# Kernel optimization log

Measured on AMD Instinct MI355X. Metric: run time of the kernel, lower is better.

## Reference

```python
import jax, jax.numpy as jnp
import numpy as np
import math

H = 128          # num heads
D = 5120         # hidden
Q_LORA = 1536
KV_LORA = 512    # nope_size / latent dim
ROPE = 64        # qk_rope_head_dim
NOPE = 128       # qk_nope_head_dim
VDIM = 128       # v_head_dim
Q_HEAD = NOPE + ROPE  # 192
EPS = 1e-6
_MSCALE = 0.1 * 1.0 * math.log(40.0) + 1.0
SCALE = (Q_HEAD ** -0.5) * _MSCALE * _MSCALE


def rmsnorm(x, w):
    var = jnp.mean(x.astype(jnp.float32) ** 2, axis=-1, keepdims=True)
    return (x * jax.lax.rsqrt(var + EPS)).astype(x.dtype) * w


def rotate_half(x):
    h = x.shape[-1] // 2
    return jnp.concatenate([-x[..., h:], x[..., :h]], axis=-1)


def apply_rope(x, cos, sin):
    return x * cos + rotate_half(x) * sin


def setup_inputs() -> dict:
    key = jax.random.key(0)
    ks = jax.random.split(key, 12)
    S = 1024
    s = 0.02
    return {
        'hidden_states': jax.random.normal(ks[0], (1, S, D), jnp.float32),
        'cos': jax.random.uniform(ks[1], (S, ROPE), jnp.float32, -1.0, 1.0),
        'sin': jax.random.uniform(ks[2], (S, ROPE), jnp.float32, -1.0, 1.0),
        'q_a_w': jax.random.normal(ks[3], (D, Q_LORA), jnp.float32) * s,
        'q_a_ln_w': jnp.ones((Q_LORA,), jnp.float32),
        'q_b_w': jax.random.normal(ks[4], (Q_LORA, H * Q_HEAD), jnp.float32) * s,
        'kv_a_w': jax.random.normal(ks[5], (D, KV_LORA + ROPE), jnp.float32) * s,
        'kv_a_ln_w': jnp.ones((KV_LORA,), jnp.float32),
        'kc_w': jax.random.normal(ks[6], (H, NOPE, KV_LORA), jnp.float32) * s,
        'vc_w': jax.random.normal(ks[7], (H, KV_LORA, VDIM), jnp.float32) * s,
        'o_w': jax.random.normal(ks[8], (H * VDIM, D), jnp.float32) * s,
    }


def reference(hidden_states, cos, sin, q_a_w, q_a_ln_w, q_b_w, kv_a_w,
              kv_a_ln_w, kc_w, vc_w, o_w):
    h = hidden_states[0]                     # [S, D]
    S = h.shape[0]

    # --- q path: low-rank q with RMSNorm, then absorbed nope proj via per-head bmm
    q = rmsnorm(h @ q_a_w, q_a_ln_w) @ q_b_w  # [S, H*192]
    q = q.reshape(S, H, Q_HEAD)
    q_nope, q_pe = q[..., :NOPE], q[..., NOPE:]         # [S,H,128], [S,H,64]
    q_nope_abs = jnp.einsum('shd,hdl->shl', q_nope, kc_w)  # [S,H,512] (kc bmm)

    # --- kv path: shared latent (MQA, 1 kv head)
    kv = h @ kv_a_w                          # [S, 512+64]
    k_pe = kv[:, KV_LORA:]                   # [S, 64]
    latent = rmsnorm(kv[:, :KV_LORA], kv_a_ln_w)  # [S, 512] = value states

    # --- partial RoPE on the 64-dim pe slice only
    q_pe = apply_rope(q_pe, cos[:, None, :], sin[:, None, :])
    k_pe = apply_rope(k_pe, cos, sin)

    q_full = jnp.concatenate([q_nope_abs, q_pe], axis=-1)  # [S,H,576]
    k_full = jnp.concatenate([latent, k_pe], axis=-1)      # [S,576]

    # --- causal MLA attention in latent space (values = 512-dim latent)
    scores = jnp.einsum('qhd,kd->hqk', q_full, k_full) * SCALE  # [H,S,S]
    causal = jnp.tril(jnp.ones((S, S), bool))
    scores = jnp.where(causal[None], scores, jnp.finfo(scores.dtype).min)
    probs = jax.nn.softmax(scores, axis=-1)
    attn = jnp.einsum('hqk,kl->qhl', probs, latent)         # [S,H,512]

    # --- vc bmm back to v_head_dim, then output proj
    out = jnp.einsum('shl,hlv->shv', attn, vc_w)            # [S,H,128]
    out = out.reshape(S, H * VDIM) @ o_w                    # [S, D]
    return out[None]                                        # [1,S,D]
```

## Files before the change

kernel.cpp:

```cpp
#include <hip/hip_runtime.h>
#include <hip/hip_bf16.h>
#include <math.h>

#define S_LEN  1024
#define DMODEL 5120
#define QLORA  1536
#define KVLORA 512
#define ROPE_D 64
#define NOPE_D 128
#define VDIM_D 128
#define QHEAD  192
#define NHEAD  128

typedef __hip_bfloat16 bf16;

using bf16x8 = __attribute__((ext_vector_type(8))) __bf16;
using f32x4  = __attribute__((ext_vector_type(4))) float;

__device__ __forceinline__ float toF(float x) { return x; }
__device__ __forceinline__ float toF(bf16 x)  { return __bfloat162float(x); }

__device__ __forceinline__ bf16x8 ld8(const bf16* p) {
  return *reinterpret_cast<const bf16x8*>(p);
}

__global__ __launch_bounds__(256) void cvt_bf16(const float* __restrict__ in,
                                                bf16* __restrict__ out) {
  const int i = (blockIdx.x * 256 + threadIdx.x) * 4;
  const float4 v = *reinterpret_cast<const float4*>(in + i);
  out[i + 0] = __float2bfloat16(v.x);
  out[i + 1] = __float2bfloat16(v.y);
  out[i + 2] = __float2bfloat16(v.z);
  out[i + 3] = __float2bfloat16(v.w);
}

__global__ __launch_bounds__(256) void transpose_w(const float* __restrict__ in,
                                                   bf16* __restrict__ out,
                                                   int R, int C) {
  __shared__ float tile[32][33];
  const int h = blockIdx.z;
  const int c0 = blockIdx.x * 32, r0 = blockIdx.y * 32;
  const int rr = threadIdx.x >> 3, cc = (threadIdx.x & 7) * 4;
  const float* ip = in + ((size_t)h * R + r0 + rr) * C + c0 + cc;
#pragma unroll
  for (int i = 0; i < 4; ++i) tile[rr][cc + i] = ip[i];
  __syncthreads();
  bf16* op = out + ((size_t)h * C + c0 + rr) * R + r0 + cc;
#pragma unroll
  for (int i = 0; i < 4; ++i) op[i] = __float2bfloat16(tile[cc + i][rr]);
}

template<int MODE, int SPLIT = 1>
__global__ __launch_bounds__(256) void gemm_mfma(const bf16* __restrict__ A,
                                                 const bf16* __restrict__ BT,
                                                 void* __restrict__ Cout,
                                                 int M, int N, int K) {
  __shared__ bf16 As[128][72];
  __shared__ bf16 Bs[128][72];
  const int n0 = blockIdx.x * 128, m0 = blockIdx.y * 128;
  const int z  = (SPLIT > 1) ? blockIdx.z : 0;
  const int Ks = K / SPLIT;
  const int kbeg = z * Ks;
  const int tid = threadIdx.x;
  const int w = tid >> 6, l = tid & 63, lr = l & 15, lg = l >> 4;
  const int wr = w >> 1, wc = w & 1;

  f32x4 acc[4][4];
#pragma unroll
  for (int x = 0; x < 4; ++x)
#pragma unroll
    for (int y = 0; y < 4; ++y) acc[x][y] = (f32x4){0.f, 0.f, 0.f, 0.f};

  for (int kk = kbeg; kk < kbeg + Ks; kk += 64) {
#pragma unroll
    for (int i = 0; i < 4; ++i) {
      const int e = tid + 256 * i;
      const int r = e >> 3, k8 = (e & 7) * 8;
      *reinterpret_cast<bf16x8*>(&As[r][k8]) =
          ld8(A + (size_t)(m0 + r) * K + kk + k8);
      const int bn = (n0 + r < N) ? n0 + r : N - 1;
      *reinterpret_cast<bf16x8*>(&Bs[r][k8]) =
          ld8(BT + (size_t)bn * K + kk + k8);
    }
    __syncthreads();
#pragma unroll
    for (int kh = 0; kh < 2; ++kh) {
      bf16x8 af[4], bg[4];
#pragma unroll
      for (int x = 0; x < 4; ++x) af[x] = ld8(&As[wr * 64 + x * 16 + lr][kh * 32 + lg * 8]);
#pragma unroll
      for (int y = 0; y < 4; ++y) bg[y] = ld8(&Bs[wc * 64 + y * 16 + lr][kh * 32 + lg * 8]);
#pragma unroll
      for (int x = 0; x < 4; ++x)
#pragma unroll
        for (int y = 0; y < 4; ++y)
          acc[x][y] = __builtin_amdgcn_mfma_f32_16x16x32_bf16(af[x], bg[y], acc[x][y], 0, 0, 0);
    }
    __syncthreads();
  }

#pragma unroll
  for (int x = 0; x < 4; ++x) {
    const int mb = m0 + wr * 64 + x * 16 + lg * 4;
#pragma unroll
    for (int y = 0; y < 4; ++y) {
      const int n = n0 + wc * 64 + y * 16 + lr;
      if (n < N) {
#pragma unroll
        for (int i = 0; i < 4; ++i) {
          const int m = mb + i;
          if (MODE == 0) {
            ((float*)Cout)[(size_t)m * N + n] = acc[x][y][i];
          } else if (MODE == 1) {
            ((bf16*)Cout)[(size_t)m * N + n] = __float2bfloat16(acc[x][y][i]);
          } else if (MODE == 2) {
            const int h = n / QHEAD, j = n - h * QHEAD;
            ((bf16*)Cout)[((size_t)h * S_LEN + m) * QHEAD + j] = __float2bfloat16(acc[x][y][i]);
          } else {
            ((float*)Cout)[(size_t)z * M * N + (size_t)m * N + n] = acc[x][y][i];
          }
        }
      }
    }
  }
}

__global__ __launch_bounds__(256) void rmsnorm_fused(const float* __restrict__ part,
                                                     const float* __restrict__ w,
                                                     bf16* __restrict__ out) {
  const int row = blockIdx.x, tid = threadIdx.x;
  __shared__ float red[256];
  float x[6];
  float ss = 0.f;
#pragma unroll
  for (int j = 0; j < 6; ++j) {
    const int c = tid + 256 * j;
    float s = 0.f;
#pragma unroll
    for (int z = 0; z < 8; ++z) s += part[((size_t)z * S_LEN + row) * QLORA + c];
    x[j] = s; ss += s * s;
  }
  red[tid] = ss; __syncthreads();
  for (int t = 128; t > 0; t >>= 1) { if (tid < t) red[tid] += red[tid + t]; __syncthreads(); }
  const float rs = rsqrtf(red[0] / (float)QLORA + 1e-6f);
#pragma unroll
  for (int j = 0; j < 6; ++j) {
    const int c = tid + 256 * j;
    out[(size_t)row * QLORA + c] = __float2bfloat16(x[j] * rs * w[c]);
  }
}

__global__ __launch_bounds__(256) void kfull_fused(const float* __restrict__ part,
                                                   const float* __restrict__ w,
                                                   const float* __restrict__ cosb,
                                                   const float* __restrict__ sinb,
                                                   bf16* __restrict__ kfull) {
  const int s = blockIdx.x, tid = threadIdx.x;
  __shared__ float red[256];
  float x0 = 0.f, x1 = 0.f;
#pragma unroll
  for (int z = 0; z < 16; ++z) {
    const float* row = part + ((size_t)z * S_LEN + s) * 576;
    x0 += row[tid]; x1 += row[256 + tid];
  }
  red[tid] = x0 * x0 + x1 * x1; __syncthreads();
  for (int t = 128; t > 0; t >>= 1) { if (tid < t) red[tid] += red[tid + t]; __syncthreads(); }
  const float rs = rsqrtf(red[0] / 512.f + 1e-6f);
  bf16* krow = kfull + (size_t)s * 576;
  krow[tid]       = __float2bfloat16(x0 * rs * w[tid]);
  krow[256 + tid] = __float2bfloat16(x1 * rs * w[256 + tid]);
  if (tid < 32) {
    const int j = tid;
    float a = 0.f, b = 0.f;
#pragma unroll
    for (int z = 0; z < 16; ++z) {
      const float* row = part + ((size_t)z * S_LEN + s) * 576;
      a += row[512 + j]; b += row[544 + j];
    }
    const float* cs = cosb + (size_t)s * 64;
    const float* sn = sinb + (size_t)s * 64;
    krow[512 + j] = __float2bfloat16(a * cs[j] - b * sn[j]);
    krow[544 + j] = __float2bfloat16(b * cs[32 + j] + a * sn[32 + j]);
  }
}

__global__ __launch_bounds__(256) void reduce2_f32(const float* __restrict__ p,
                                                   float* __restrict__ out) {
  const size_t i = ((size_t)blockIdx.x * 256 + threadIdx.x) * 4;
  const float4 a = *reinterpret_cast<const float4*>(p + i);
  const float4 b = *reinterpret_cast<const float4*>(p + (size_t)S_LEN * DMODEL + i);
  float4 r; r.x = a.x + b.x; r.y = a.y + b.y; r.z = a.z + b.z; r.w = a.w + b.w;
  *reinterpret_cast<float4*>(out + i) = r;
}

__global__ __launch_bounds__(256) void rope_q_kernel(bf16* __restrict__ qperm,
                                                     const float* __restrict__ cosb,
                                                     const float* __restrict__ sinb) {
  const int idx = blockIdx.x * 256 + threadIdx.x;
  const int h = idx >> 15;
  const int rem = idx & 32767;
  const int s = rem >> 5;
  const int j = rem & 31;
  bf16* base = qperm + ((size_t)h * S_LEN + s) * QHEAD + NOPE_D;
  const float a = toF(base[j]), b = toF(base[32 + j]);
  const float* cs = cosb + (size_t)s * 64;
  const float* sn = sinb + (size_t)s * 64;
  base[j]      = __float2bfloat16(a * cs[j] - b * sn[j]);
  base[32 + j] = __float2bfloat16(b * cs[32 + j] + a * sn[32 + j]);
}

__global__ __launch_bounds__(256) void latT_kernel(const bf16* __restrict__ kfull,
                                                   bf16* __restrict__ latT) {
  const int gid = blockIdx.x * 256 + threadIdx.x;
  const int v = gid >> 10, s = gid & 1023;
  latT[gid] = kfull[(size_t)s * 576 + v];
}

#define QB 32
__global__ __launch_bounds__(256, 3) void attn_mfma(const bf16* __restrict__ qperm,
                                                    const bf16* __restrict__ kfull,
                                                    const bf16* __restrict__ kcT,
                                                    const bf16* __restrict__ vcT,
                                                    const bf16* __restrict__ latT,
                                                    bf16* __restrict__ attnv,
                                                    float scale) {
  const int bi = blockIdx.x;
  const int y  = bi >> 3;
  const int h  = (bi & 7) * 16 + (y >> 5);
  const int qb = y & 31;
  const int r0 = qb * QB;
  const int tid = threadIdx.x;
  const int w = tid >> 6, l = tid & 63, lr = l & 15, lg = l >> 4;

  __shared__ bf16  Qf[QB][584];
  __shared__ float St[QB][68];
  __shared__ bf16  Pt[QB][72];
  __shared__ float mrow[QB], lrow[QB], arow[QB];

  for (int e = tid; e < QB * 64; e += 256) {
    const int i = e >> 6, j = e & 63;
    Qf[i][512 + j] = qperm[((size_t)h * S_LEN + r0 + i) * QHEAD + NOPE_D + j];
  }
  {
    bf16x8 qn[2][4];
#pragma unroll
    for (int x = 0; x < 2; ++x) {
      const bf16* qp = qperm + ((size_t)h * S_LEN + r0 + x * 16 + lr) * QHEAD;
#pragma unroll
      for (int t = 0; t < 4; ++t) qn[x][t] = ld8(qp + t * 32 + lg * 8);
    }
#pragma unroll
    for (int ff = 0; ff < 2; ++ff) {
      bf16x8 kb[4][4];
#pragma unroll
      for (int f4 = 0; f4 < 4; ++f4) {
        const int col = w * 128 + (ff * 4 + f4) * 16 + lr;
        const bf16* kp = kcT + ((size_t)h * 512 + col) * 128 + lg * 8;
#pragma unroll
        for (int t = 0; t < 4; ++t) kb[f4][t] = ld8(kp + t * 32);
      }
#pragma unroll
      for (int f4 = 0; f4 < 4; ++f4) {
        f32x4 a0 = {0.f, 0.f, 0.f, 0.f}, a1 = {0.f, 0.f, 0.f, 0.f};
        const int col = w * 128 + (ff * 4 + f4) * 16 + lr;
#pragma unroll
        for (int t = 0; t < 4; ++t) {
          a0 = __builtin_amdgcn_mfma_f32_16x16x32_bf16(qn[0][t], kb[f4][t], a0, 0, 0, 0);
          a1 = __builtin_amdgcn_mfma_f32_16x16x32_bf16(qn[1][t], kb[f4][t], a1, 0, 0, 0);
        }
#pragma unroll
        for (int i = 0; i < 4; ++i) {
          Qf[lg * 4 + i][col]      = __float2bfloat16(a0[i]);
          Qf[16 + lg * 4 + i][col] = __float2bfloat16(a1[i]);
        }
      }
    }
  }
  if (tid < QB) { mrow[tid] = -INFINITY; lrow[tid] = 0.f; }
  __syncthreads();

  f32x4 o[2][8];
#pragma unroll
  for (int x = 0; x < 2; ++x)
#pragma unroll
    for (int f = 0; f < 8; ++f) o[x][f] = (f32x4){0.f, 0.f, 0.f, 0.f};

  const int kend = r0 + QB;
  for (int k0 = 0; k0 < kend; k0 += 64) {
    {
      const int key = k0 + w * 16 + lr;
      const bf16* kp = kfull + (size_t)key * 576 + lg * 8;
      bf16x8 bb[18];
#pragma unroll
      for (int t = 0; t < 18; ++t) bb[t] = ld8(kp + t * 32);
      f32x4 s0 = {0.f, 0.f, 0.f, 0.f}, s1 = {0.f, 0.f, 0.f, 0.f};
      __builtin_amdgcn_s_setprio(1);
#pragma unroll
      for (int t = 0; t < 18; ++t) {
        s0 = __builtin_amdgcn_mfma_f32_16x16x32_bf16(ld8(&Qf[lr][t * 32 + lg * 8]), bb[t], s0, 0, 0, 0);
        s1 = __builtin_amdgcn_mfma_f32_16x16x32_bf16(ld8(&Qf[16 + lr][t * 32 + lg * 8]), bb[t], s1, 0, 0, 0);
      }
      __builtin_amdgcn_s_setprio(0);
#pragma unroll
      for (int i = 0; i < 4; ++i) {
        const int q0 = r0 + lg * 4 + i;
        const int q1 = r0 + 16 + lg * 4 + i;
        St[lg * 4 + i][w * 16 + lr]      = (key <= q0) ? s0[i] * scale : -INFINITY;
        St[16 + lg * 4 + i][w * 16 + lr] = (key <= q1) ? s1[i] * scale : -INFINITY;
      }
    }
    __syncthreads();
    {
      const int r = tid >> 3, seg = tid & 7;
      const float4 v0 = *reinterpret_cast<const float4*>(&St[r][seg * 8]);
      const float4 v1 = *reinterpret_cast<const float4*>(&St[r][seg * 8 + 4]);
      float mx = fmaxf(fmaxf(fmaxf(v0.x, v0.y), fmaxf(v0.z, v0.w)),
                       fmaxf(fmaxf(v1.x, v1.y), fmaxf(v1.z, v1.w)));
#pragma unroll
      for (int m = 1; m < 8; m <<= 1) mx = fmaxf(mx, __shfl_xor(mx, m, 64));
      const float mold = mrow[r];
      const float mnew = fmaxf(mold, mx);
      const float p0 = expf(v0.x - mnew), p1 = expf(v0.y - mnew);
      const float p2 = expf(v0.z - mnew), p3 = expf(v0.w - mnew);
      const float p4 = expf(v1.x - mnew), p5 = expf(v1.y - mnew);
      const float p6 = expf(v1.z - mnew), p7 = expf(v1.w - mnew);
      Pt[r][seg * 8 + 0] = __float2bfloat16(p0);
      Pt[r][seg * 8 + 1] = __float2bfloat16(p1);
      Pt[r][seg * 8 + 2] = __float2bfloat16(p2);
      Pt[r][seg * 8 + 3] = __float2bfloat16(p3);
      Pt[r][seg * 8 + 4] = __float2bfloat16(p4);
      Pt[r][seg * 8 + 5] = __float2bfloat16(p5);
      Pt[r][seg * 8 + 6] = __float2bfloat16(p6);
      Pt[r][seg * 8 + 7] = __float2bfloat16(p7);
      float sum = p0 + p1 + p2 + p3 + p4 + p5 + p6 + p7;
#pragma unroll
      for (int m = 1; m < 8; m <<= 1) sum += __shfl_xor(sum, m, 64);
      if (seg == 0) {
        const float alpha = expf(mold - mnew);
        lrow[r] = lrow[r] * alpha + sum;
        mrow[r] = mnew;
        arow[r] = alpha;
      }
    }
    __syncthreads();
    {
      bf16x8 bl[16];
#pragma unroll
      for (int f = 0; f < 8; ++f) {
        const int v = w * 128 + f * 16 + lr;
        const bf16* bp = latT + (size_t)v * S_LEN + k0 + lg * 8;
        bl[2 * f]     = ld8(bp);
        bl[2 * f + 1] = ld8(bp + 32);
      }
      float al0[4], al1[4];
#pragma unroll
      for (int i = 0; i < 4; ++i) {
        al0[i] = arow[lg * 4 + i];
        al1[i] = arow[16 + lg * 4 + i];
      }
#pragma unroll
      for (int f = 0; f < 8; ++f)
#pragma unroll
        for (int i = 0; i < 4; ++i) {
          o[0][f][i] *= al0[i];
          o[1][f][i] *= al1[i];
        }
      bf16x8 pa[2][2];
      pa[0][0] = ld8(&Pt[lr][lg * 8]);
      pa[0][1] = ld8(&Pt[lr][32 + lg * 8]);
      pa[1][0] = ld8(&Pt[16 + lr][lg * 8]);
      pa[1][1] = ld8(&Pt[16 + lr][32 + lg * 8]);
      __builtin_amdgcn_s_setprio(1);
#pragma unroll
      for (int f = 0; f < 8; ++f) {
        o[0][f] = __builtin_amdgcn_mfma_f32_16x16x32_bf16(pa[0][0], bl[2 * f],     o[0][f], 0, 0, 0);
        o[0][f] = __builtin_amdgcn_mfma_f32_16x16x32_bf16(pa[0][1], bl[2 * f + 1], o[0][f], 0, 0, 0);
        o[1][f] = __builtin_amdgcn_mfma_f32_16x16x32_bf16(pa[1][0], bl[2 * f],     o[1][f], 0, 0, 0);
        o[1][f] = __builtin_amdgcn_mfma_f32_16x16x32_bf16(pa[1][1], bl[2 * f + 1], o[1][f], 0, 0, 0);
      }
      __builtin_amdgcn_s_setprio(0);
    }
  }

  {
    float li0[4], li1[4];
#pragma unroll
    for (int i = 0; i < 4; ++i) {
      li0[i] = 1.f / lrow[lg * 4 + i];
      li1[i] = 1.f / lrow[16 + lg * 4 + i];
    }
#pragma unroll
    for (int f = 0; f < 8; ++f) {
      const int v = w * 128 + f * 16 + lr;
#pragma unroll
      for (int i = 0; i < 4; ++i) {
        Qf[lg * 4 + i][v]      = __float2bfloat16(o[0][f][i] * li0[i]);
        Qf[16 + lg * 4 + i][v] = __float2bfloat16(o[1][f][i] * li1[i]);
      }
    }
  }
  __syncthreads();
#pragma unroll
  for (int cf = 0; cf < 2; ++cf) {
    const int c = w * 32 + cf * 16 + lr;
    const bf16* vp = vcT + ((size_t)h * 128 + c) * 512 + lg * 8;
    bf16x8 vb[16];
#pragma unroll
    for (int kt = 0; kt < 16; ++kt) vb[kt] = ld8(vp + kt * 32);
    f32x4 acc0 = {0.f, 0.f, 0.f, 0.f}, acc1 = {0.f, 0.f, 0.f, 0.f};
#pragma unroll
    for (int kt = 0; kt < 16; ++kt) {
      acc0 = __builtin_amdgcn_mfma_f32_16x16x32_bf16(ld8(&Qf[lr][kt * 32 + lg * 8]), vb[kt], acc0, 0, 0, 0);
      acc1 = __builtin_amdgcn_mfma_f32_16x16x32_bf16(ld8(&Qf[16 + lr][kt * 32 + lg * 8]), vb[kt], acc1, 0, 0, 0);
    }
#pragma unroll
    for (int i = 0; i < 4; ++i) {
      attnv[(size_t)(r0 + lg * 4 + i) * (NHEAD * VDIM_D) + h * VDIM_D + c]      = __float2bfloat16(acc0[i]);
      attnv[(size_t)(r0 + 16 + lg * 4 + i) * (NHEAD * VDIM_D) + h * VDIM_D + c] = __float2bfloat16(acc1[i]);
    }
  }
}

extern "C" void kernel_launch(void* const* d_in, const int* in_sizes, int n_in,
                              void* d_out, int out_size, void* d_ws, size_t ws_size,
                              hipStream_t stream) {
  const float* hidden    = (const float*)d_in[0];
  const float* cosb      = (const float*)d_in[1];
  const float* sinb      = (const float*)d_in[2];
  const float* q_a_w     = (const float*)d_in[3];
  const float* q_a_ln_w  = (const float*)d_in[4];
  const float* q_b_w     = (const float*)d_in[5];
  const float* kv_a_w    = (const float*)d_in[6];
  const float* kv_a_ln_w = (const float*)d_in[7];
  const float* kc_w      = (const float*)d_in[8];
  const float* vc_w      = (const float*)d_in[9];
  const float* o_w       = (const float*)d_in[10];
  float* out = (float*)d_out;

  char* ws = (char*)d_ws;
  bf16*  attnv   = (bf16*)(ws + 0);
  bf16*  kcT     = (bf16*)(ws + 33554432);
  bf16*  vcT     = (bf16*)(ws + 50331648);
  bf16*  kfull   = (bf16*)(ws + 67108864);
  bf16*  latT    = (bf16*)(ws + 68288512);
  bf16*  qan     = (bf16*)(ws + 69337088);
  bf16*  hb      = (bf16*)(ws + 72482816);
  bf16*  qaT     = (bf16*)(ws + 82968576);
  bf16*  kvaT    = (bf16*)(ws + 98697216);
  bf16*  qperm   = (bf16*)(ws + 104595456);
  float* qa_part = (float*)(ws + 104595456);
  bf16*  qbT     = (bf16*)(ws + 154927104);
  float* kv_part = (float*)(ws + 154927104);
  float* o_part  = (float*)(ws + 33554432);
  bf16*  owT     = (bf16*)(ws + 75497472);

  const double msc = 0.1 * log(40.0) + 1.0;
  const float scale = (float)(pow((double)QHEAD, -0.5) * msc * msc);

  cvt_bf16<<<(S_LEN * DMODEL) / 1024, 256, 0, stream>>>(hidden, hb);
  transpose_w<<<dim3(QLORA / 32, DMODEL / 32, 1), 256, 0, stream>>>(q_a_w, qaT, DMODEL, QLORA);
  transpose_w<<<dim3(576 / 32, DMODEL / 32, 1), 256, 0, stream>>>(kv_a_w, kvaT, DMODEL, 576);
  transpose_w<<<dim3((NHEAD * QHEAD) / 32, QLORA / 32, 1), 256, 0, stream>>>(q_b_w, qbT, QLORA, NHEAD * QHEAD);
  transpose_w<<<dim3(512 / 32, 128 / 32, NHEAD), 256, 0, stream>>>(kc_w, kcT, 128, 512);
  transpose_w<<<dim3(128 / 32, 512 / 32, NHEAD), 256, 0, stream>>>(vc_w, vcT, 512, 128);

  gemm_mfma<3, 8><<<dim3(QLORA / 128, S_LEN / 128, 8), 256, 0, stream>>>(
      hb, qaT, qa_part, S_LEN, QLORA, DMODEL);
  rmsnorm_fused<<<S_LEN, 256, 0, stream>>>(qa_part, q_a_ln_w, qan);
  gemm_mfma<2><<<dim3((NHEAD * QHEAD) / 128, S_LEN / 128), 256, 0, stream>>>(
      qan, qbT, qperm, S_LEN, NHEAD * QHEAD, QLORA);
  gemm_mfma<3, 16><<<dim3(5, S_LEN / 128, 16), 256, 0, stream>>>(
      hb, kvaT, kv_part, S_LEN, KVLORA + ROPE_D, DMODEL);
  kfull_fused<<<S_LEN, 256, 0, stream>>>(kv_part, kv_a_ln_w, cosb, sinb, kfull);
  latT_kernel<<<(KVLORA * S_LEN) / 256, 256, 0, stream>>>(kfull, latT);
  rope_q_kernel<<<(NHEAD * S_LEN * 32) / 256, 256, 0, stream>>>(qperm, cosb, sinb);
  attn_mfma<<<dim3(NHEAD * (S_LEN / QB)), 256, 0, stream>>>(
      qperm, kfull, kcT, vcT, latT, attnv, scale);
  transpose_w<<<dim3(DMODEL / 32, (NHEAD * VDIM_D) / 32, 1), 256, 0, stream>>>(
      o_w, owT, NHEAD * VDIM_D, DMODEL);
  gemm_mfma<3, 2><<<dim3(DMODEL / 128, S_LEN / 128, 2), 256, 0, stream>>>(
      attnv, owT, o_part, S_LEN, DMODEL, NHEAD * VDIM_D);
  reduce2_f32<<<(S_LEN * DMODEL) / 1024, 256, 0, stream>>>(o_part, out);
}
```

Before: 2.039 ms.

## Process 128 keys per softmax step and merge score/prob buffers in LDS

The attention loop now handles 128 keys per iteration (two 64-key score halves) before each online-softmax update, which halves the number of softmax passes and barrier pairs per key range. Probabilities are written back as fp32 into the score buffer and packed to bf16 at PV time, and the row statistics are stored in spare columns of that buffer. Latent values are loaded in 32-key chunks with early exit at the causal boundary. The cost is a larger LDS score buffer, an extra barrier at the end of each iteration, some wasted masked work on the final partial block, and possible register pressure changes.

```diff
diff --git a/kernel.cpp b/kernel.cpp
--- a/kernel.cpp
+++ b/kernel.cpp
@@ -22,6 +22,17 @@
 
 __device__ __forceinline__ bf16x8 ld8(const bf16* p) {
   return *reinterpret_cast<const bf16x8*>(p);
+}
+
+__device__ __forceinline__ bf16x8 pack8(const float* p) {
+  const float4 a = *reinterpret_cast<const float4*>(p);
+  const float4 b = *reinterpret_cast<const float4*>(p + 4);
+  union { bf16x8 v; bf16 e[8]; } u;
+  u.e[0] = __float2bfloat16(a.x); u.e[1] = __float2bfloat16(a.y);
+  u.e[2] = __float2bfloat16(a.z); u.e[3] = __float2bfloat16(a.w);
+  u.e[4] = __float2bfloat16(b.x); u.e[5] = __float2bfloat16(b.y);
+  u.e[6] = __float2bfloat16(b.z); u.e[7] = __float2bfloat16(b.w);
+  return u.v;
 }
 
 __global__ __launch_bounds__(256) void cvt_bf16(const float* __restrict__ in,
@@ -233,9 +244,7 @@
   const int w = tid >> 6, l = tid & 63, lr = l & 15, lg = l >> 4;
 
   __shared__ bf16  Qf[QB][584];
-  __shared__ float St[QB][68];
-  __shared__ bf16  Pt[QB][72];
-  __shared__ float mrow[QB], lrow[QB], arow[QB];
+  __shared__ float St[QB][132];
 
   for (int e = tid; e < QB * 64; e += 256) {
     const int i = e >> 6, j = e & 63;
@@ -276,7 +285,7 @@
       }
     }
   }
-  if (tid < QB) { mrow[tid] = -INFINITY; lrow[tid] = 0.f; }
+  if (tid < QB) { St[tid][128] = -INFINITY; St[tid][129] = 0.f; }
   __syncthreads();
 
   f32x4 o[2][8];
@@ -286,77 +295,79 @@
     for (int f = 0; f < 8; ++f) o[x][f] = (f32x4){0.f, 0.f, 0.f, 0.f};
 
   const int kend = r0 + QB;
-  for (int k0 = 0; k0 < kend; k0 += 64) {
-    {
-      const int key = k0 + w * 16 + lr;
-      const bf16* kp = kfull + (size_t)key * 576 + lg * 8;
-      bf16x8 bb[18];
-#pragma unroll
-      for (int t = 0; t < 18; ++t) bb[t] = ld8(kp + t * 32);
-      f32x4 s0 = {0.f, 0.f, 0.f, 0.f}, s1 = {0.f, 0.f, 0.f, 0.f};
-      __builtin_amdgcn_s_setprio(1);
-#pragma unroll
-      for (int t = 0; t < 18; ++t) {
-        s0 = __builtin_amdgcn_mfma_f32_16x16x32_bf16(ld8(&Qf[lr][t * 32 + lg * 8]), bb[t], s0, 0, 0, 0);
-        s1 = __builtin_amdgcn_mfma_f32_16x16x32_bf16(ld8(&Qf[16 + lr][t * 32 + lg * 8]), bb[t], s1, 0, 0, 0);
-      }
-      __builtin_amdgcn_s_setprio(0);
-#pragma unroll
-      for (int i = 0; i < 4; ++i) {
-        const int q0 = r0 + lg * 4 + i;
-        const int q1 = r0 + 16 + lg * 4 + i;
-        St[lg * 4 + i][w * 16 + lr]      = (key <= q0) ? s0[i] * scale : -INFINITY;
-        St[16 + lg * 4 + i][w * 16 + lr] = (key <= q1) ? s1[i] * scale : -INFINITY;
+  for (int k0 = 0; k0 < kend; k0 += 128) {
+#pragma unroll
+    for (int half = 0; half < 2; ++half) {
+      const int kbase = k0 + half * 64;
+      if (kbase < kend) {
+        const int key = kbase + w * 16 + lr;
+        const bf16* kp = kfull + (size_t)key * 576 + lg * 8;
+        bf16x8 bb[18];
+#pragma unroll
+        for (int t = 0; t < 18; ++t) bb[t] = ld8(kp + t * 32);
+        f32x4 s0 = {0.f, 0.f, 0.f, 0.f}, s1 = {0.f, 0.f, 0.f, 0.f};
+        __builtin_amdgcn_s_setprio(1);
+#pragma unroll
+        for (int t = 0; t < 18; ++t) {
+          s0 = __builtin_amdgcn_mfma_f32_16x16x32_bf16(ld8(&Qf[lr][t * 32 + lg * 8]), bb[t], s0, 0, 0, 0);
+          s1 = __builtin_amdgcn_mfma_f32_16x16x32_bf16(ld8(&Qf[16 + lr][t * 32 + lg * 8]), bb[t], s1, 0, 0, 0);
+        }
+        __builtin_amdgcn_s_setprio(0);
+#pragma unroll
+        for (int i = 0; i < 4; ++i) {
+          const int q0 = r0 + lg * 4 + i;
+          const int q1 = r0 + 16 + lg * 4 + i;
+          St[lg * 4 + i][half * 64 + w * 16 + lr]      = (key <= q0) ? s0[i] * scale : -INFINITY;
+          St[16 + lg * 4 + i][half * 64 + w * 16 + lr] = (key <= q1) ? s1[i] * scale : -INFINITY;
+        }
+      } else {
+#pragma unroll
+        for (int i = 0; i < 4; ++i) {
+          St[lg * 4 + i][half * 64 + w * 16 + lr]      = -INFINITY;
+          St[16 + lg * 4 + i][half * 64 + w * 16 + lr] = -INFINITY;
+        }
       }
     }
     __syncthreads();
     {
       const int r = tid >> 3, seg = tid & 7;
-      const float4 v0 = *reinterpret_cast<const float4*>(&St[r][seg * 8]);
-      const float4 v1 = *reinterpret_cast<const float4*>(&St[r][seg * 8 + 4]);
-      float mx = fmaxf(fmaxf(fmaxf(v0.x, v0.y), fmaxf(v0.z, v0.w)),
-                       fmaxf(fmaxf(v1.x, v1.y), fmaxf(v1.z, v1.w)));
+      float v[16];
+#pragma unroll
+      for (int j = 0; j < 4; ++j) {
+        const float4 t4 = *reinterpret_cast<const float4*>(&St[r][seg * 16 + 4 * j]);
+        v[4 * j + 0] = t4.x; v[4 * j + 1] = t4.y; v[4 * j + 2] = t4.z; v[4 * j + 3] = t4.w;
+      }
+      float mx = v[0];
+#pragma unroll
+      for (int j = 1; j < 16; ++j) mx = fmaxf(mx, v[j]);
 #pragma unroll
       for (int m = 1; m < 8; m <<= 1) mx = fmaxf(mx, __shfl_xor(mx, m, 64));
-      const float mold = mrow[r];
+      const float mold = St[r][128];
       const float mnew = fmaxf(mold, mx);
-      const float p0 = expf(v0.x - mnew), p1 = expf(v0.y - mnew);
-      const float p2 = expf(v0.z - mnew), p3 = expf(v0.w - mnew);
-      const float p4 = expf(v1.x - mnew), p5 = expf(v1.y - mnew);
-      const float p6 = expf(v1.z - mnew), p7 = expf(v1.w - mnew);
-      Pt[r][seg * 8 + 0] = __float2bfloat16(p0);
-      Pt[r][seg * 8 + 1] = __float2bfloat16(p1);
-      Pt[r][seg * 8 + 2] = __float2bfloat16(p2);
-      Pt[r][seg * 8 + 3] = __float2bfloat16(p3);
-      Pt[r][seg * 8 + 4] = __float2bfloat16(p4);
-      Pt[r][seg * 8 + 5] = __float2bfloat16(p5);
-      Pt[r][seg * 8 + 6] = __float2bfloat16(p6);
-      Pt[r][seg * 8 + 7] = __float2bfloat16(p7);
-      float sum = p0 + p1 + p2 + p3 + p4 + p5 + p6 + p7;
+      float sum = 0.f;
+#pragma unroll
+      for (int j = 0; j < 16; ++j) { v[j] = expf(v[j] - mnew); sum += v[j]; }
+#pragma unroll
+      for (int j = 0; j < 4; ++j) {
+        float4 t4; t4.x = v[4 * j]; t4.y = v[4 * j + 1]; t4.z = v[4 * j + 2]; t4.w = v[4 * j + 3];
+        *reinterpret_cast<float4*>(&St[r][seg * 16 + 4 * j]) = t4;
+      }
 #pragma unroll
       for (int m = 1; m < 8; m <<= 1) sum += __shfl_xor(sum, m, 64);
       if (seg == 0) {
         const float alpha = expf(mold - mnew);
-        lrow[r] = lrow[r] * alpha + sum;
-        mrow[r] = mnew;
-        arow[r] = alpha;
+        St[r][129] = St[r][129] * alpha + sum;
+        St[r][128] = mnew;
+        St[r][130] = alpha;
       }
     }
     __syncthreads();
     {
-      bf16x8 bl[16];
-#pragma unroll
-      for (int f = 0; f < 8; ++f) {
-        const int v = w * 128 + f * 16 + lr;
-        const bf16* bp = latT + (size_t)v * S_LEN + k0 + lg * 8;
-        bl[2 * f]     = ld8(bp);
-        bl[2 * f + 1] = ld8(bp + 32);
-      }
       float al0[4], al1[4];
 #pragma unroll
       for (int i = 0; i < 4; ++i) {
-        al0[i] = arow[lg * 4 + i];
-        al1[i] = arow[16 + lg * 4 + i];
+        al0[i] = St[lg * 4 + i][130];
+        al1[i] = St[16 + lg * 4 + i][130];
       }
 #pragma unroll
       for (int f = 0; f < 8; ++f)
@@ -365,29 +376,35 @@
           o[0][f][i] *= al0[i];
           o[1][f][i] *= al1[i];
         }
-      bf16x8 pa[2][2];
-      pa[0][0] = ld8(&Pt[lr][lg * 8]);
-      pa[0][1] = ld8(&Pt[lr][32 + lg * 8]);
-      pa[1][0] = ld8(&Pt[16 + lr][lg * 8]);
-      pa[1][1] = ld8(&Pt[16 + lr][32 + lg * 8]);
-      __builtin_amdgcn_s_setprio(1);
-#pragma unroll
-      for (int f = 0; f < 8; ++f) {
-        o[0][f] = __builtin_amdgcn_mfma_f32_16x16x32_bf16(pa[0][0], bl[2 * f],     o[0][f], 0, 0, 0);
-        o[0][f] = __builtin_amdgcn_mfma_f32_16x16x32_bf16(pa[0][1], bl[2 * f + 1], o[0][f], 0, 0, 0);
-        o[1][f] = __builtin_amdgcn_mfma_f32_16x16x32_bf16(pa[1][0], bl[2 * f],     o[1][f], 0, 0, 0);
-        o[1][f] = __builtin_amdgcn_mfma_f32_16x16x32_bf16(pa[1][1], bl[2 * f + 1], o[1][f], 0, 0, 0);
-      }
-      __builtin_amdgcn_s_setprio(0);
-    }
+#pragma unroll
+      for (int c = 0; c < 4; ++c) {
+        if (k0 + c * 32 >= kend) break;
+        const bf16x8 pa0 = pack8(&St[lr][c * 32 + lg * 8]);
+        const bf16x8 pa1 = pack8(&St[16 + lr][c * 32 + lg * 8]);
+        bf16x8 bl[8];
+#pragma unroll
+        for (int f = 0; f < 8; ++f) {
+          const int v = w * 128 + f * 16 + lr;
+          bl[f] = ld8(latT + (size_t)v * S_LEN + k0 + c * 32 + lg * 8);
+        }
+        __builtin_amdgcn_s_setprio(1);
+#pragma unroll
+        for (int f = 0; f < 8; ++f) {
+          o[0][f] = __builtin_amdgcn_mfma_f32_16x16x32_bf16(pa0, bl[f], o[0][f], 0, 0, 0);
+          o[1][f] = __builtin_amdgcn_mfma_f32_16x16x32_bf16(pa1, bl[f], o[1][f], 0, 0, 0);
+        }
+        __builtin_amdgcn_s_setprio(0);
+      }
+    }
+    __syncthreads();
   }
 
   {
     float li0[4], li1[4];
 #pragma unroll
     for (int i = 0; i < 4; ++i) {
-      li0[i] = 1.f / lrow[lg * 4 + i];
-      li1[i] = 1.f / lrow[16 + lg * 4 + i];
+      li0[i] = 1.f / St[lg * 4 + i][129];
+      li1[i] = 1.f / St[16 + lg * 4 + i][129];
     }
 #pragma unroll
     for (int f = 0; f < 8; ++f) {
```

After: 2.085 ms. +2.2%, slower.
